# Kernel tuning notes

Hardware: AMD Instinct MI355X
Metric: run time of the kernel (lower is better)

## Reference

```python
import jax, jax.numpy as jnp
import numpy as np

N_C, N_M, E = 200000, 50000, 1000000
D, H, O = 64, 64, 2


def _seg_mean(msgs, idx, n):
    # mean aggregation as in PyG SAGEConv default; nodes with no in-edges get 0
    s = jax.ops.segment_sum(msgs, idx, num_segments=n)
    c = jax.ops.segment_sum(jnp.ones((msgs.shape[0], 1), msgs.dtype), idx, num_segments=n)
    return s / jnp.maximum(c, 1.0)


def _sage(x_src, x_dst, src, dst, n_dst, Wl, Wr, b):
    agg = _seg_mean(x_src[src], dst, n_dst)  # gather + scatter-mean
    return agg @ Wl + x_dst @ Wr + b


def setup_inputs():
    key = jax.random.key(0)
    ks = jax.random.split(key, 20)

    def lin(k, i, o):
        return (jax.random.normal(k, (i, o), jnp.float32) / np.sqrt(i).astype(np.float32))

    d = {}
    d["x_c"] = jax.random.normal(ks[0], (N_C, D), jnp.float32)
    d["x_m"] = jax.random.normal(ks[1], (N_M, D), jnp.float32)
    d["cm_src"] = jax.random.randint(ks[2], (E,), 0, N_C, jnp.int32)
    d["cm_dst"] = jax.random.randint(ks[3], (E,), 0, N_M, jnp.int32)
    d["mc_src"] = jax.random.randint(ks[4], (E,), 0, N_M, jnp.int32)
    d["mc_dst"] = jax.random.randint(ks[5], (E,), 0, N_C, jnp.int32)
    # layer 1 (per edge type: neighbor weight Wl, root weight Wr, bias)
    d["Wl1_cm"] = lin(ks[6], D, H); d["Wr1_cm"] = lin(ks[7], D, H); d["b1_cm"] = jnp.zeros((H,), jnp.float32)
    d["Wl1_mc"] = lin(ks[8], D, H); d["Wr1_mc"] = lin(ks[9], D, H); d["b1_mc"] = jnp.zeros((H,), jnp.float32)
    # layer 2
    d["Wl2_cm"] = lin(ks[10], H, H); d["Wr2_cm"] = lin(ks[11], H, H); d["b2_cm"] = jnp.zeros((H,), jnp.float32)
    d["Wl2_mc"] = lin(ks[12], H, H); d["Wr2_mc"] = lin(ks[13], H, H); d["b2_mc"] = jnp.zeros((H,), jnp.float32)
    # final linear on customer nodes
    d["W_lin"] = lin(ks[14], H, O); d["b_lin"] = jnp.zeros((O,), jnp.float32)
    return d


def reference(x_c, x_m, cm_src, cm_dst, mc_src, mc_dst,
              Wl1_cm, Wr1_cm, b1_cm, Wl1_mc, Wr1_mc, b1_mc,
              Wl2_cm, Wr2_cm, b2_cm, Wl2_mc, Wr2_mc, b2_mc,
              W_lin, b_lin):
    # conv1: hetero SAGE, aggr='sum' across edge types (one per dst type here)
    h_m = _sage(x_c, x_m, cm_src, cm_dst, N_M, Wl1_cm, Wr1_cm, b1_cm)
    h_c = _sage(x_m, x_c, mc_src, mc_dst, N_C, Wl1_mc, Wr1_mc, b1_mc)
    h_m = jax.nn.relu(h_m)
    h_c = jax.nn.relu(h_c)
    # conv2
    h2_m = _sage(h_c, h_m, cm_src, cm_dst, N_M, Wl2_cm, Wr2_cm, b2_cm)
    h2_c = _sage(h_m, h_c, mc_src, mc_dst, N_C, Wl2_mc, Wr2_mc, b2_mc)
    # final linear on customer nodes (h2_m unused, as in original module)
    del h2_m
    return h2_c @ W_lin + b_lin
```

## Files before the change

kernel.cpp:

```cpp
#include <hip/hip_runtime.h>

#define NC 200000
#define NM 50000
#define NE 1000000
#define DF 64

#define BSH_M 8
#define BW_M 256
#define NBM ((NM + BW_M - 1) >> BSH_M)
#define BSH_C 10
#define BW_C 1024
#define NBC ((NC + BW_C - 1) >> BSH_C)
#define CH 4096
#define NSB ((NE + CH - 1) / CH)
#define PSB 1024

typedef __attribute__((ext_vector_type(8))) short bf16x8;
typedef __attribute__((ext_vector_type(4))) float f32x4;
typedef __attribute__((ext_vector_type(4))) unsigned short u16x4;

__device__ __forceinline__ short bf16rn(float x) {
    unsigned u = __builtin_bit_cast(unsigned, x);
    unsigned r = u + 0x7FFFu + ((u >> 16) & 1u);
    return (short)(r >> 16);
}
__device__ __forceinline__ float bf16f(short h) {
    unsigned u = ((unsigned)(unsigned short)h) << 16;
    return __builtin_bit_cast(float, u);
}
__device__ __forceinline__ void split8(const f32x4 u, const f32x4 v,
                                       bf16x8& hi, bf16x8& lo) {
#pragma unroll
    for (int b = 0; b < 4; ++b) {
        short h = bf16rn(u[b]);
        hi[b] = h;
        lo[b] = bf16rn(u[b] - bf16f(h));
    }
#pragma unroll
    for (int b = 0; b < 4; ++b) {
        short h = bf16rn(v[b]);
        hi[4 + b] = h;
        lo[4 + b] = bf16rn(v[b] - bf16f(h));
    }
}

__device__ __forceinline__ int wscan_incl(int v, int lane) {
#pragma unroll
    for (int off = 1; off < 64; off <<= 1) {
        int y = __shfl_up(v, off);
        if (lane >= off) v += y;
    }
    return v;
}

__global__ __launch_bounds__(256) void prep_k(const int* __restrict__ cm_dst,
                                              const int* __restrict__ mc_dst,
                                              int* __restrict__ pmM,
                                              int* __restrict__ pmC,
                                              const float* __restrict__ x_c,
                                              const float* __restrict__ x_m,
                                              u16x4* __restrict__ xc16,
                                              u16x4* __restrict__ xm16,
                                              const float* __restrict__ Wl2,
                                              const float* __restrict__ Wr2,
                                              const float* __restrict__ b2,
                                              const float* __restrict__ Wlin,
                                              const float* __restrict__ blin,
                                              float* __restrict__ Vl,
                                              float* __restrict__ Vr,
                                              float* __restrict__ bo) {
    __shared__ int cnt[256];
    const int t = threadIdx.x;
    if (blockIdx.x < 2 * NSB) {
        const int side = (blockIdx.x >= NSB);
        const int blk = blockIdx.x - side * NSB;
        const int* dst = side ? mc_dst : cm_dst;
        int* pm = side ? pmC : pmM;
        const int nb = side ? NBC : NBM;
        const int bsh = side ? BSH_C : BSH_M;
        cnt[t] = 0;
        __syncthreads();
        const int e0 = blk * CH;
        const int n = min(CH, NE - e0);
        for (int i = t; i < n; i += 256) atomicAdd(&cnt[dst[e0 + i] >> bsh], 1);
        __syncthreads();
        if (t < nb) pm[(long)blk * nb + t] = cnt[t];
    } else if (blockIdx.x < 2 * NSB + PSB) {
        const int blk = blockIdx.x - 2 * NSB;
        const int NC4 = NC * (DF / 4);
        const int NT4 = (NC + NM) * (DF / 4);
        const int st = PSB * 256;
        for (int i = blk * 256 + t; i < NT4; i += st) {
            const bool isc = (i < NC4);
            const int j = isc ? i : i - NC4;
            const f32x4 v = isc ? ((const f32x4*)x_c)[j] : ((const f32x4*)x_m)[j];
            u16x4 o;
#pragma unroll
            for (int b = 0; b < 4; ++b) o[b] = (unsigned short)bf16rn(v[b]);
            if (isc) xc16[j] = o;
            else     xm16[j] = o;
        }
    } else {
        for (int i = t; i < 2 * 64 * 16; i += 256) {
            float* dst = (i < 1024) ? Vl : Vr;
            dst[i & 1023] = 0.0f;
        }
        __syncthreads();
        if (t < 128) {
            const int k = t >> 1, o = t & 1;
            float sl = 0.f, sr = 0.f;
            for (int j = 0; j < 64; ++j) {
                sl += Wl2[k * 64 + j] * Wlin[j * 2 + o];
                sr += Wr2[k * 64 + j] * Wlin[j * 2 + o];
            }
            Vl[k * 16 + o] = sl;
            Vr[k * 16 + o] = sr;
        }
        if (t < 2) {
            float s = blin[t];
            for (int j = 0; j < 64; ++j) s += b2[j] * Wlin[j * 2 + t];
            bo[t] = s;
        }
    }
}

__global__ __launch_bounds__(256) void cred2_k(const int* __restrict__ pmM,
                                               const int* __restrict__ pmC,
                                               int* __restrict__ totM,
                                               int* __restrict__ totC) {
    __shared__ int red[256];
    const int side = (blockIdx.x >= NBM);
    const int b = blockIdx.x - side * NBM;
    const int* pm = side ? pmC : pmM;
    const int nb = side ? NBC : NBM;
    int* tot = side ? totC : totM;
    const int t = threadIdx.x;
    int s = 0;
    for (int i = t; i < NSB; i += 256) s += pm[(long)i * nb + b];
    red[t] = s;
    __syncthreads();
    for (int off = 128; off > 0; off >>= 1) {
        if (t < off) red[t] += red[t + off];
        __syncthreads();
    }
    if (t == 0) tot[b] = red[0];
}

__global__ __launch_bounds__(256) void cscan3_k(const int* __restrict__ totM,
                                                const int* __restrict__ totC,
                                                int* __restrict__ cstartM,
                                                int* __restrict__ cstartC,
                                                int* __restrict__ ccurM,
                                                int* __restrict__ ccurC) {
    __shared__ int wsum[4];
    const int t = threadIdx.x, lane = t & 63, wv = t >> 6;
    int s = (t < NBM) ? totM[t] : 0;
    int incl = wscan_incl(s, lane);
    if (lane == 63) wsum[wv] = incl;
    __syncthreads();
    int wadd = 0;
#pragma unroll
    for (int w = 0; w < 4; ++w) wadd += (w < wv) ? wsum[w] : 0;
    const int tot = incl + wadd;
    if (t < NBM) { cstartM[t] = tot - s; ccurM[t] = tot - s; }
    if (t == NBM - 1) cstartM[NBM] = tot;
    __syncthreads();
    int s2 = (t < NBC) ? totC[t] : 0;
    int incl2 = wscan_incl(s2, lane);
    if (lane == 63) wsum[wv] = incl2;
    __syncthreads();
    int wadd2 = 0;
#pragma unroll
    for (int w = 0; w < 4; ++w) wadd2 += (w < wv) ? wsum[w] : 0;
    const int tot2 = incl2 + wadd2;
    if (t < NBC) { cstartC[t] = tot2 - s2; ccurC[t] = tot2 - s2; }
    if (t == NBC - 1) cstartC[NBC] = tot2;
}

__global__ __launch_bounds__(256) void bsort2_k(const int* __restrict__ cm_src,
                                                const int* __restrict__ cm_dst,
                                                const int* __restrict__ mc_src,
                                                const int* __restrict__ mc_dst,
                                                const int* __restrict__ pmM,
                                                const int* __restrict__ pmC,
                                                int* __restrict__ ccurM,
                                                int* __restrict__ ccurC,
                                                int* __restrict__ bktM,
                                                int* __restrict__ bktC) {
    __shared__ int cnt[256], pfx[256], gbase[256];
    __shared__ int wsum[4];
    __shared__ int stage[CH];
    const int side = (blockIdx.x >= NSB);
    const int blk = blockIdx.x - side * NSB;
    const int* src = side ? mc_src : cm_src;
    const int* dst = side ? mc_dst : cm_dst;
    const int* pm = side ? pmC : pmM;
    int* ccur = side ? ccurC : ccurM;
    int* bkt = side ? bktC : bktM;
    const int nb = side ? NBC : NBM;
    const int bsh = side ? BSH_C : BSH_M;
    const int bmask = (side ? BW_C : BW_M) - 1;

    const int t = threadIdx.x, lane = t & 63, wv = t >> 6;
    const int e0 = blk * CH;
    const int n = min(CH, NE - e0);
    const int myc = (t < nb) ? pm[(long)blk * nb + t] : 0;
    int incl = wscan_incl(myc, lane);
    if (lane == 63) wsum[wv] = incl;
    __syncthreads();
    int wadd = 0;
#pragma unroll
    for (int w = 0; w < 4; ++w) wadd += (w < wv) ? wsum[w] : 0;
    const int excl = wadd + incl - myc;
    if (t < nb && myc > 0) gbase[t] = atomicAdd(&ccur[t], myc);
    pfx[t] = excl;
    cnt[t] = 0;
    __syncthreads();
    for (int i = t; i < n; i += 256) {
        const int d = dst[e0 + i];
        const int b = d >> bsh;
        const int p = pfx[b] + atomicAdd(&cnt[b], 1);
        stage[p] = (src[e0 + i] << bsh) | (d & bmask);
    }
    __syncthreads();
    for (int b = wv; b < nb; b += 4) {
        const int c = cnt[b];
        if (c == 0) continue;
        const int gb = gbase[b], lo = pfx[b];
        for (int j = lane; j < c; j += 64) bkt[gb + j] = stage[lo + j];
    }
}

__global__ __launch_bounds__(256) void bp22_k(const int* __restrict__ bktM,
                                              const int* __restrict__ cstartM,
                                              int* __restrict__ startM,
                                              int* __restrict__ srtM,
                                              const int* __restrict__ bktC,
                                              const int* __restrict__ cstartC,
                                              int* __restrict__ startC,
                                              int* __restrict__ srtC) {
    __shared__ int lcur[BW_C];
    __shared__ int wsum[4];
    const int side = (blockIdx.x >= NBM);
    const int blk = blockIdx.x - side * NBM;
    const int* bkt = side ? bktC : bktM;
    const int* cstart = side ? cstartC : cstartM;
    int* start = side ? startC : startM;
    int* srt = side ? srtC : srtM;
    const int n_nodes = side ? NC : NM;
    const int bw = side ? BW_C : BW_M;
    const int bsh = side ? BSH_C : BSH_M;
    const int base = blk << bsh;
    const int t = threadIdx.x, lane = t & 63, wv = t >> 6;

    const int e0 = cstart[blk];
    const int e1 = cstart[blk + 1];

    for (int i = t; i < bw; i += 256) lcur[i] = 0;
    __syncthreads();
    for (int e = e0 + t; e < e1; e += 256) atomicAdd(&lcur[bkt[e] & (bw - 1)], 1);
    __syncthreads();

    int c0 = 0, c1 = 0, c2 = 0, c3 = 0;
    const bool act = (4 * t < bw);
    if (act) {
        c0 = lcur[4 * t + 0]; c1 = lcur[4 * t + 1];
        c2 = lcur[4 * t + 2]; c3 = lcur[4 * t + 3];
    }
    const int local = c0 + c1 + c2 + c3;
    int incl = wscan_incl(local, lane);
    if (lane == 63) wsum[wv] = incl;
    __syncthreads();
    int wadd = 0;
#pragma unroll
    for (int w = 0; w < 4; ++w) wadd += (w < wv) ? wsum[w] : 0;
    const int p0 = e0 + wadd + incl - local;
    const int p1 = p0 + c0, p2 = p1 + c1, p3 = p2 + c2;
    if (act) {
        lcur[4 * t + 0] = p0;
        lcur[4 * t + 1] = p1;
        lcur[4 * t + 2] = p2;
        lcur[4 * t + 3] = p3;
        if (base + 4 * t + 0 < n_nodes) start[base + 4 * t + 0] = p0;
        if (base + 4 * t + 1 < n_nodes) start[base + 4 * t + 1] = p1;
        if (base + 4 * t + 2 < n_nodes) start[base + 4 * t + 2] = p2;
        if (base + 4 * t + 3 < n_nodes) start[base + 4 * t + 3] = p3;
    }
    if (t == 0 && base + bw >= n_nodes) start[n_nodes] = e1;
    __syncthreads();

    for (int e = e0 + t; e < e1; e += 256) {
        const int p = bkt[e];
        const int pos = atomicAdd(&lcur[p & (bw - 1)], 1);
        srt[pos] = p >> bsh;
    }
}

__device__ __forceinline__ void agg_node16(const unsigned short* __restrict__ xhi,
                                           const int* __restrict__ start,
                                           const int* __restrict__ srt,
                                           unsigned short* __restrict__ mean16,
                                           int n, int k4) {
    const int s0 = start[n], s1 = start[n + 1];
    f32x4 a0 = {0.f, 0.f, 0.f, 0.f}, a1 = {0.f, 0.f, 0.f, 0.f};
    f32x4 a2 = {0.f, 0.f, 0.f, 0.f}, a3 = {0.f, 0.f, 0.f, 0.f};
    int e = s0;
    for (; e + 3 < s1; e += 4) {
        const int i0 = srt[e + 0], i1 = srt[e + 1];
        const int i2 = srt[e + 2], i3 = srt[e + 3];
        const u16x4 v0 = *(const u16x4*)(xhi + (long)i0 * DF + k4);
        const u16x4 v1 = *(const u16x4*)(xhi + (long)i1 * DF + k4);
        const u16x4 v2 = *(const u16x4*)(xhi + (long)i2 * DF + k4);
        const u16x4 v3 = *(const u16x4*)(xhi + (long)i3 * DF + k4);
#pragma unroll
        for (int c = 0; c < 4; ++c) {
            a0[c] += bf16f((short)v0[c]);
            a1[c] += bf16f((short)v1[c]);
            a2[c] += bf16f((short)v2[c]);
            a3[c] += bf16f((short)v3[c]);
        }
    }
    for (; e < s1; ++e) {
        const int i0 = srt[e];
        const u16x4 v0 = *(const u16x4*)(xhi + (long)i0 * DF + k4);
#pragma unroll
        for (int c = 0; c < 4; ++c) a0[c] += bf16f((short)v0[c]);
    }
    const float inv = 1.0f / fmaxf((float)(s1 - s0), 1.0f);
    u16x4 o;
#pragma unroll
    for (int c = 0; c < 4; ++c)
        o[c] = (unsigned short)bf16rn(((a0[c] + a1[c]) + (a2[c] + a3[c])) * inv);
    *(u16x4*)(mean16 + (long)n * DF + k4) = o;
}

__global__ __launch_bounds__(256) void aggall_k(const unsigned short* __restrict__ xc16,
                                                const int* __restrict__ startM,
                                                const int* __restrict__ srt_cm,
                                                unsigned short* __restrict__ aggm16,
                                                const unsigned short* __restrict__ xm16,
                                                const int* __restrict__ startC,
                                                const int* __restrict__ srt_mc,
                                                unsigned short* __restrict__ meanx16) {
    const int t = threadIdx.x;
    const int sg = t >> 4;
    const int k4 = (t & 15) * 4;
    if (blockIdx.x < NM / 16) {
        const int n = blockIdx.x * 16 + sg;
        agg_node16(xc16, startM, srt_cm, aggm16, n, k4);
    } else {
        const int n = (blockIdx.x - NM / 16) * 16 + sg;
        agg_node16(xm16, startC, srt_mc, meanx16, n, k4);
    }
}

__global__ __launch_bounds__(256) void aggz_k(const float2* __restrict__ zm,
                                              const int* __restrict__ start,
                                              const int* __restrict__ srt,
                                              float2* __restrict__ meanz, int n_nodes) {
    int n = blockIdx.x * blockDim.x + threadIdx.x;
    const int st = gridDim.x * blockDim.x;
    for (; n < n_nodes; n += st) {
        const int s0 = start[n], s1 = start[n + 1];
        float z0 = 0.f, z1 = 0.f, y0 = 0.f, y1 = 0.f;
        int e = s0;
        for (; e + 1 < s1; e += 2) {
            const float2 a = zm[srt[e]];
            const float2 b = zm[srt[e + 1]];
            z0 += a.x; z1 += a.y;
            y0 += b.x; y1 += b.y;
        }
        if (e < s1) {
            const float2 a = zm[srt[e]];
            z0 += a.x; z1 += a.y;
        }
        const float inv = 1.0f / fmaxf((float)(s1 - s0), 1.0f);
        float2 o = {(z0 + y0) * inv, (z1 + y1) * inv};
        meanz[n] = o;
    }
}

#define MFMA(a, b, c) __builtin_amdgcn_mfma_f32_16x16x32_bf16((a), (b), (c), 0, 0, 0)

#define LOAD_W(Wl, Wr, col, g, wlh, wll, wrh, wrl)          \
    do {                                                    \
        _Pragma("unroll")                                   \
        for (int q = 0; q < 2; ++q) {                       \
            f32x4 tl0, tl1, tr0, tr1;                       \
            _Pragma("unroll")                               \
            for (int b = 0; b < 4; ++b) {                   \
                int k = 32 * q + 8 * (g) + b;               \
                tl0[b] = (Wl)[k * DF + (col)];              \
                tr0[b] = (Wr)[k * DF + (col)];              \
                tl1[b] = (Wl)[(k + 4) * DF + (col)];        \
                tr1[b] = (Wr)[(k + 4) * DF + (col)];        \
            }                                               \
            split8(tl0, tl1, wlh[q], wll[q]);               \
            split8(tr0, tr1, wrh[q], wrl[q]);               \
        }                                                   \
    } while (0)

#define LOAD_V(V, col, g, vh, vlo)                          \
    do {                                                    \
        _Pragma("unroll")                                   \
        for (int q = 0; q < 2; ++q) {                       \
            f32x4 t0, t1;                                   \
            _Pragma("unroll")                               \
            for (int b = 0; b < 4; ++b) {                   \
                int k = 32 * q + 8 * (g) + b;               \
                t0[b] = (V)[k * 16 + (col)];                \
                t1[b] = (V)[(k + 4) * 16 + (col)];          \
            }                                               \
            split8(t0, t1, vh[q], vlo[q]);                  \
        }                                                   \
    } while (0)

__global__ __launch_bounds__(256) void dense1nm_k(const unsigned short* __restrict__ mean16,
                                                  const unsigned short* __restrict__ xm16,
                                                  const float* __restrict__ Wl,
                                                  const float* __restrict__ Wr,
                                                  const float* __restrict__ bias,
                                                  const float* __restrict__ Vl,
                                                  float* __restrict__ zm,
                                                  int n_nodes) {
    __shared__ float sZ[2][4][16][2];
    const int t = threadIdx.x;
    const int lane = t & 63;
    const int wv = t >> 6;
    const int col = wv * 16 + (lane & 15);
    const int g = lane >> 4;

    bf16x8 wlh[2], wll[2], wrh[2], wrl[2];
    LOAD_W(Wl, Wr, col, g, wlh, wll, wrh, wrl);
    const float bv = bias[col];
    const float vl0 = Vl[col * 16 + 0];
    const float vl1 = Vl[col * 16 + 1];

    const int nrt = n_nodes >> 4;
    int par = 0;
    for (int rt = blockIdx.x; rt < nrt; rt += gridDim.x, par ^= 1) {
        const long rowA = (long)rt * 16 + (lane & 15);
        const bf16x8 m0 = *(const bf16x8*)(mean16 + rowA * DF + 8 * g);
        const bf16x8 m1 = *(const bf16x8*)(mean16 + rowA * DF + 32 + 8 * g);
        const bf16x8 x0 = *(const bf16x8*)(xm16 + rowA * DF + 8 * g);
        const bf16x8 x1 = *(const bf16x8*)(xm16 + rowA * DF + 32 + 8 * g);
        f32x4 acc = {0.f, 0.f, 0.f, 0.f};
        acc = MFMA(m0, wlh[0], acc);
        acc = MFMA(m0, wll[0], acc);
        acc = MFMA(m1, wlh[1], acc);
        acc = MFMA(m1, wll[1], acc);
        acc = MFMA(x0, wrh[0], acc);
        acc = MFMA(x0, wrl[0], acc);
        acc = MFMA(x1, wrh[1], acc);
        acc = MFMA(x1, wrl[1], acc);

        float z0[4], z1[4];
#pragma unroll
        for (int r = 0; r < 4; ++r) {
            const float h = fmaxf(acc[r] + bv, 0.0f);
            z0[r] = h * vl0;
            z1[r] = h * vl1;
        }
#pragma unroll
        for (int m = 1; m < 16; m <<= 1) {
#pragma unroll
            for (int r = 0; r < 4; ++r) {
                z0[r] += __shfl_xor(z0[r], m);
                z1[r] += __shfl_xor(z1[r], m);
            }
        }
        if ((lane & 15) == 0) {
#pragma unroll
            for (int r = 0; r < 4; ++r) {
                sZ[par][wv][4 * g + r][0] = z0[r];
                sZ[par][wv][4 * g + r][1] = z1[r];
            }
        }
        __syncthreads();
        if (t < 16) {
            const long node = (long)rt * 16 + t;
            const float a = sZ[par][0][t][0] + sZ[par][1][t][0] +
                            sZ[par][2][t][0] + sZ[par][3][t][0];
            const float b = sZ[par][0][t][1] + sZ[par][1][t][1] +
                            sZ[par][2][t][1] + sZ[par][3][t][1];
            zm[node * 2 + 0] = a;
            zm[node * 2 + 1] = b;
        }
    }
}

__global__ __launch_bounds__(256) void densec_k(const unsigned short* __restrict__ meanx,
                                                const float* __restrict__ meanz,
                                                const unsigned short* __restrict__ xc,
                                                const float* __restrict__ Wl1,
                                                const float* __restrict__ Wr1,
                                                const float* __restrict__ b1,
                                                const float* __restrict__ Vr,
                                                const float* __restrict__ bo,
                                                float* __restrict__ out, int n_nodes) {
    __shared__ unsigned short sH[2][16][72];
    const int t = threadIdx.x;
    const int lane = t & 63;
    const int wv = t >> 6;
    const int col = wv * 16 + (lane & 15);
    const int g = lane >> 4;

    bf16x8 w1lh[2], w1ll[2], w1rh[2], w1rl[2];
    LOAD_W(Wl1, Wr1, col, g, w1lh, w1ll, w1rh, w1rl);
    const float bv1 = b1[col];
    bf16x8 vrh[2], vrl[2];
    LOAD_V(Vr, (lane & 15), g, vrh, vrl);
    const int oc = lane & 15;
    const float bo2 = (oc < 2) ? bo[oc] : 0.0f;

    const int nrt = n_nodes >> 4;
    int par = 0;
    for (int rt = blockIdx.x; rt < nrt; rt += gridDim.x, par ^= 1) {
        const long rowA = (long)rt * 16 + (lane & 15);
        const bf16x8 mx0 = *(const bf16x8*)(meanx + rowA * DF + 8 * g);
        const bf16x8 mx1 = *(const bf16x8*)(meanx + rowA * DF + 32 + 8 * g);
        const bf16x8 xc0 = *(const bf16x8*)(xc + rowA * DF + 8 * g);
        const bf16x8 xc1 = *(const bf16x8*)(xc + rowA * DF + 32 + 8 * g);
        float mzv[4];
        if (oc < 2) {
#pragma unroll
            for (int r = 0; r < 4; ++r)
                mzv[r] = meanz[((long)rt * 16 + 4 * g + r) * 2 + oc];
        }

        f32x4 acc = {0.f, 0.f, 0.f, 0.f};
        acc = MFMA(mx0, w1lh[0], acc);
        acc = MFMA(mx0, w1ll[0], acc);
        acc = MFMA(mx1, w1lh[1], acc);
        acc = MFMA(mx1, w1ll[1], acc);
        acc = MFMA(xc0, w1rh[0], acc);
        acc = MFMA(xc0, w1rl[0], acc);
        acc = MFMA(xc1, w1rh[1], acc);
        acc = MFMA(xc1, w1rl[1], acc);
#pragma unroll
        for (int r = 0; r < 4; ++r)
            sH[par][4 * g + r][col] = (unsigned short)bf16rn(fmaxf(acc[r] + bv1, 0.0f));
        __syncthreads();

        const bf16x8 hc0 = *(const bf16x8*)&sH[par][lane & 15][8 * g];
        const bf16x8 hc1 = *(const bf16x8*)&sH[par][lane & 15][32 + 8 * g];
        f32x4 a2 = {0.f, 0.f, 0.f, 0.f};
        a2 = MFMA(hc0, vrh[0], a2);
        a2 = MFMA(hc0, vrl[0], a2);
        a2 = MFMA(hc1, vrh[1], a2);
        a2 = MFMA(hc1, vrl[1], a2);
        if (oc < 2) {
#pragma unroll
            for (int r = 0; r < 4; ++r) {
                const long node = (long)rt * 16 + 4 * g + r;
                out[node * 2 + oc] = a2[r] + mzv[r] + bo2;
            }
        }
    }
}

extern "C" void kernel_launch(void* const* d_in, const int* in_sizes, int n_in,
                              void* d_out, int out_size, void* d_ws, size_t ws_size,
                              hipStream_t stream) {
    const float* x_c = (const float*)d_in[0];
    const float* x_m = (const float*)d_in[1];
    const int* cm_src = (const int*)d_in[2];
    const int* cm_dst = (const int*)d_in[3];
    const int* mc_src = (const int*)d_in[4];
    const int* mc_dst = (const int*)d_in[5];
    const float* Wl1_cm = (const float*)d_in[6];
    const float* Wr1_cm = (const float*)d_in[7];
    const float* b1_cm = (const float*)d_in[8];
    const float* Wl1_mc = (const float*)d_in[9];
    const float* Wr1_mc = (const float*)d_in[10];
    const float* b1_mc = (const float*)d_in[11];
    const float* Wl2_mc = (const float*)d_in[15];
    const float* Wr2_mc = (const float*)d_in[16];
    const float* b2_mc = (const float*)d_in[17];
    const float* W_lin = (const float*)d_in[18];
    const float* b_lin = (const float*)d_in[19];
    float* out = (float*)d_out;

    unsigned short* up = (unsigned short*)d_ws;
    unsigned short* aggm16 = up;
    unsigned short* xm16 = aggm16 + (long)NM * DF;
    unsigned short* xc16 = xm16 + (long)NM * DF;
    unsigned short* meanx16 = xc16 + (long)NC * DF;
    float* zm = (float*)(meanx16 + (long)NC * DF);
    float* meanz = zm + (long)NM * 2;
    float* Vl = meanz + (long)NC * 2;
    float* Vr = Vl + 64 * 16;
    float* bo = Vr + 64 * 16;
    int* ip = (int*)(bo + 4);

    int* startM = ip;
    int* startC = startM + (NM + 1);
    int* cstartM = startC + (NC + 1);
    int* cstartC = cstartM + (NBM + 1);
    int* ccurM = cstartC + (NBC + 1);
    int* ccurC = ccurM + NBM;
    int* totM = ccurC + NBC;
    int* totC = totM + NBM;
    int* pmM = totC + NBC;
    int* pmC = pmM + NSB * NBM;
    int* srt_cm = pmC + NSB * NBC;
    int* srt_mc = srt_cm + NE;
    int* bktM = srt_mc + NE;
    int* bktC = bktM + NE;

    prep_k<<<2 * NSB + PSB + 1, 256, 0, stream>>>(cm_dst, mc_dst, pmM, pmC,
                                                  x_c, x_m, (u16x4*)xc16, (u16x4*)xm16,
                                                  Wl2_mc, Wr2_mc, b2_mc, W_lin, b_lin,
                                                  Vl, Vr, bo);
    cred2_k<<<NBM + NBC, 256, 0, stream>>>(pmM, pmC, totM, totC);
    cscan3_k<<<1, 256, 0, stream>>>(totM, totC, cstartM, cstartC, ccurM, ccurC);
    bsort2_k<<<2 * NSB, 256, 0, stream>>>(cm_src, cm_dst, mc_src, mc_dst,
                                          pmM, pmC, ccurM, ccurC, bktM, bktC);
    bp22_k<<<NBM + NBC, 256, 0, stream>>>(bktM, cstartM, startM, srt_cm,
                                          bktC, cstartC, startC, srt_mc);

    aggall_k<<<NM / 16 + NC / 16, 256, 0, stream>>>(xc16, startM, srt_cm, aggm16,
                                                    xm16, startC, srt_mc, meanx16);

    dense1nm_k<<<1024, 256, 0, stream>>>(aggm16, xm16, Wl1_cm, Wr1_cm, b1_cm,
                                         Vl, zm, NM);

    aggz_k<<<782, 256, 0, stream>>>((const float2*)zm, startC, srt_mc,
                                    (float2*)meanz, NC);

    densec_k<<<2048, 256, 0, stream>>>(meanx16, meanz, xc16,
                                       Wl1_mc, Wr1_mc, b1_mc,
                                       Vr, bo, out, NC);
}
```

Baseline: 170.2 us.

## Fuse merchant aggregation with layer-1 dense projection via shared memory

Merchant-side mean aggregation now writes its bf16 rows into a shared-memory tile, and the same block immediately runs the MFMA dense layer-1 projection that produces zm. This removes the aggm16 global buffer round trip and one kernel launch. In exchange, each merchant block reloads and splits the weight matrices for a single 16-row tile instead of amortizing them across many tiles, and adds a block barrier.

```diff
diff --git a/kernel.cpp b/kernel.cpp
--- a/kernel.cpp
+++ b/kernel.cpp
@@ -299,7 +299,7 @@
 __device__ __forceinline__ void agg_node16(const unsigned short* __restrict__ xhi,
                                            const int* __restrict__ start,
                                            const int* __restrict__ srt,
-                                           unsigned short* __restrict__ mean16,
+                                           unsigned short* __restrict__ dstRow,
                                            int n, int k4) {
     const int s0 = start[n], s1 = start[n + 1];
     f32x4 a0 = {0.f, 0.f, 0.f, 0.f}, a1 = {0.f, 0.f, 0.f, 0.f};
@@ -331,53 +331,7 @@
 #pragma unroll
     for (int c = 0; c < 4; ++c)
         o[c] = (unsigned short)bf16rn(((a0[c] + a1[c]) + (a2[c] + a3[c])) * inv);
-    *(u16x4*)(mean16 + (long)n * DF + k4) = o;
-}
-
-__global__ __launch_bounds__(256) void aggall_k(const unsigned short* __restrict__ xc16,
-                                                const int* __restrict__ startM,
-                                                const int* __restrict__ srt_cm,
-                                                unsigned short* __restrict__ aggm16,
-                                                const unsigned short* __restrict__ xm16,
-                                                const int* __restrict__ startC,
-                                                const int* __restrict__ srt_mc,
-                                                unsigned short* __restrict__ meanx16) {
-    const int t = threadIdx.x;
-    const int sg = t >> 4;
-    const int k4 = (t & 15) * 4;
-    if (blockIdx.x < NM / 16) {
-        const int n = blockIdx.x * 16 + sg;
-        agg_node16(xc16, startM, srt_cm, aggm16, n, k4);
-    } else {
-        const int n = (blockIdx.x - NM / 16) * 16 + sg;
-        agg_node16(xm16, startC, srt_mc, meanx16, n, k4);
-    }
-}
-
-__global__ __launch_bounds__(256) void aggz_k(const float2* __restrict__ zm,
-                                              const int* __restrict__ start,
-                                              const int* __restrict__ srt,
-                                              float2* __restrict__ meanz, int n_nodes) {
-    int n = blockIdx.x * blockDim.x + threadIdx.x;
-    const int st = gridDim.x * blockDim.x;
-    for (; n < n_nodes; n += st) {
-        const int s0 = start[n], s1 = start[n + 1];
-        float z0 = 0.f, z1 = 0.f, y0 = 0.f, y1 = 0.f;
-        int e = s0;
-        for (; e + 1 < s1; e += 2) {
-            const float2 a = zm[srt[e]];
-            const float2 b = zm[srt[e + 1]];
-            z0 += a.x; z1 += a.y;
-            y0 += b.x; y1 += b.y;
-        }
-        if (e < s1) {
-            const float2 a = zm[srt[e]];
-            z0 += a.x; z1 += a.y;
-        }
-        const float inv = 1.0f / fmaxf((float)(s1 - s0), 1.0f);
-        float2 o = {(z0 + y0) * inv, (z1 + y1) * inv};
-        meanz[n] = o;
-    }
+    *(u16x4*)(dstRow + k4) = o;
 }
 
 #define MFMA(a, b, c) __builtin_amdgcn_mfma_f32_16x16x32_bf16((a), (b), (c), 0, 0, 0)
@@ -415,33 +369,41 @@
         }                                                   \
     } while (0)
 
-__global__ __launch_bounds__(256) void dense1nm_k(const unsigned short* __restrict__ mean16,
-                                                  const unsigned short* __restrict__ xm16,
-                                                  const float* __restrict__ Wl,
-                                                  const float* __restrict__ Wr,
-                                                  const float* __restrict__ bias,
-                                                  const float* __restrict__ Vl,
-                                                  float* __restrict__ zm,
-                                                  int n_nodes) {
-    __shared__ float sZ[2][4][16][2];
+__global__ __launch_bounds__(256) void aggall2_k(const unsigned short* __restrict__ xc16,
+                                                 const int* __restrict__ startM,
+                                                 const int* __restrict__ srt_cm,
+                                                 const unsigned short* __restrict__ xm16,
+                                                 const float* __restrict__ Wl,
+                                                 const float* __restrict__ Wr,
+                                                 const float* __restrict__ bias,
+                                                 const float* __restrict__ Vl,
+                                                 float* __restrict__ zm,
+                                                 const int* __restrict__ startC,
+                                                 const int* __restrict__ srt_mc,
+                                                 unsigned short* __restrict__ meanx16) {
     const int t = threadIdx.x;
-    const int lane = t & 63;
-    const int wv = t >> 6;
-    const int col = wv * 16 + (lane & 15);
-    const int g = lane >> 4;
-
-    bf16x8 wlh[2], wll[2], wrh[2], wrl[2];
-    LOAD_W(Wl, Wr, col, g, wlh, wll, wrh, wrl);
-    const float bv = bias[col];
-    const float vl0 = Vl[col * 16 + 0];
-    const float vl1 = Vl[col * 16 + 1];
-
-    const int nrt = n_nodes >> 4;
-    int par = 0;
-    for (int rt = blockIdx.x; rt < nrt; rt += gridDim.x, par ^= 1) {
-        const long rowA = (long)rt * 16 + (lane & 15);
-        const bf16x8 m0 = *(const bf16x8*)(mean16 + rowA * DF + 8 * g);
-        const bf16x8 m1 = *(const bf16x8*)(mean16 + rowA * DF + 32 + 8 * g);
+    const int sg = t >> 4;
+    const int k4 = (t & 15) * 4;
+    if (blockIdx.x < NM / 16) {
+        __shared__ unsigned short sM[16][72];
+        __shared__ float sZ[4][16][2];
+        const int base = blockIdx.x * 16;
+        agg_node16(xc16, startM, srt_cm, &sM[sg][0], base + sg, k4);
+        __syncthreads();
+
+        const int lane = t & 63;
+        const int wv = t >> 6;
+        const int col = wv * 16 + (lane & 15);
+        const int g = lane >> 4;
+        bf16x8 wlh[2], wll[2], wrh[2], wrl[2];
+        LOAD_W(Wl, Wr, col, g, wlh, wll, wrh, wrl);
+        const float bv = bias[col];
+        const float vl0 = Vl[col * 16 + 0];
+        const float vl1 = Vl[col * 16 + 1];
+
+        const bf16x8 m0 = *(const bf16x8*)&sM[lane & 15][8 * g];
+        const bf16x8 m1 = *(const bf16x8*)&sM[lane & 15][32 + 8 * g];
+        const long rowA = (long)base + (lane & 15);
         const bf16x8 x0 = *(const bf16x8*)(xm16 + rowA * DF + 8 * g);
         const bf16x8 x1 = *(const bf16x8*)(xm16 + rowA * DF + 32 + 8 * g);
         f32x4 acc = {0.f, 0.f, 0.f, 0.f};
@@ -472,20 +434,47 @@
         if ((lane & 15) == 0) {
 #pragma unroll
             for (int r = 0; r < 4; ++r) {
-                sZ[par][wv][4 * g + r][0] = z0[r];
-                sZ[par][wv][4 * g + r][1] = z1[r];
+                sZ[wv][4 * g + r][0] = z0[r];
+                sZ[wv][4 * g + r][1] = z1[r];
             }
         }
         __syncthreads();
         if (t < 16) {
-            const long node = (long)rt * 16 + t;
-            const float a = sZ[par][0][t][0] + sZ[par][1][t][0] +
-                            sZ[par][2][t][0] + sZ[par][3][t][0];
-            const float b = sZ[par][0][t][1] + sZ[par][1][t][1] +
-                            sZ[par][2][t][1] + sZ[par][3][t][1];
+            const long node = (long)base + t;
+            const float a = sZ[0][t][0] + sZ[1][t][0] + sZ[2][t][0] + sZ[3][t][0];
+            const float b2 = sZ[0][t][1] + sZ[1][t][1] + sZ[2][t][1] + sZ[3][t][1];
             zm[node * 2 + 0] = a;
-            zm[node * 2 + 1] = b;
-        }
+            zm[node * 2 + 1] = b2;
+        }
+    } else {
+        const int n = (blockIdx.x - NM / 16) * 16 + sg;
+        agg_node16(xm16, startC, srt_mc, meanx16 + (long)n * DF, n, k4);
+    }
+}
+
+__global__ __launch_bounds__(256) void aggz_k(const float2* __restrict__ zm,
+                                              const int* __restrict__ start,
+                                              const int* __restrict__ srt,
+                                              float2* __restrict__ meanz, int n_nodes) {
+    int n = blockIdx.x * blockDim.x + threadIdx.x;
+    const int st = gridDim.x * blockDim.x;
+    for (; n < n_nodes; n += st) {
+        const int s0 = start[n], s1 = start[n + 1];
+        float z0 = 0.f, z1 = 0.f, y0 = 0.f, y1 = 0.f;
+        int e = s0;
+        for (; e + 1 < s1; e += 2) {
+            const float2 a = zm[srt[e]];
+            const float2 b = zm[srt[e + 1]];
+            z0 += a.x; z1 += a.y;
+            y0 += b.x; y1 += b.y;
+        }
+        if (e < s1) {
+            const float2 a = zm[srt[e]];
+            z0 += a.x; z1 += a.y;
+        }
+        const float inv = 1.0f / fmaxf((float)(s1 - s0), 1.0f);
+        float2 o = {(z0 + y0) * inv, (z1 + y1) * inv};
+        meanz[n] = o;
     }
 }
 
@@ -582,8 +571,7 @@
     float* out = (float*)d_out;
 
     unsigned short* up = (unsigned short*)d_ws;
-    unsigned short* aggm16 = up;
-    unsigned short* xm16 = aggm16 + (long)NM * DF;
+    unsigned short* xm16 = up;
     unsigned short* xc16 = xm16 + (long)NM * DF;
     unsigned short* meanx16 = xc16 + (long)NC * DF;
     float* zm = (float*)(meanx16 + (long)NC * DF);
@@ -619,11 +607,9 @@
     bp22_k<<<NBM + NBC, 256, 0, stream>>>(bktM, cstartM, startM, srt_cm,
                                           bktC, cstartC, startC, srt_mc);
 
-    aggall_k<<<NM / 16 + NC / 16, 256, 0, stream>>>(xc16, startM, srt_cm, aggm16,
-                                                    xm16, startC, srt_mc, meanx16);
-
-    dense1nm_k<<<1024, 256, 0, stream>>>(aggm16, xm16, Wl1_cm, Wr1_cm, b1_cm,
-                                         Vl, zm, NM);
+    aggall2_k<<<NM / 16 + NC / 16, 256, 0, stream>>>(xc16, startM, srt_cm,
+                                                     xm16, Wl1_cm, Wr1_cm, b1_cm, Vl, zm,
+                                                     startC, srt_mc, meanx16);
 
     aggz_k<<<782, 256, 0, stream>>>((const float2*)zm, startC, srt_mc,
                                     (float2*)meanz, NC);
```

After: 176.8 us. 3.9% more time.
